# Performance work log

Measured on AMD Instinct MI355X. Metric: run time of the kernel, lower is better.

Reference implementation:

```python
import jax, jax.numpy as jnp
import numpy as np

NUM_HEADS = 16
HIDDEN = 1024
ATTN_DIM = 64            # per-head q/k dim
HEAD_OUT = 64            # per-head v dim
OUT_DIM = 1024
BATCH, SEQ = 2, 2048


def setup_inputs() -> dict:
    key = jax.random.key(0)
    ks = jax.random.split(key, 9)
    s_in = 1.0 / np.sqrt(HIDDEN)
    s_o = 1.0 / np.sqrt(NUM_HEADS * HEAD_OUT)
    return {
        "x": jax.random.normal(ks[0], (BATCH, SEQ, HIDDEN), dtype=jnp.float32),
        # Linear weights stored [in, out] so y = x @ W + b
        "Wq": jax.random.uniform(ks[1], (HIDDEN, NUM_HEADS * ATTN_DIM), jnp.float32, -s_in, s_in),
        "bq": jax.random.uniform(ks[2], (NUM_HEADS * ATTN_DIM,), jnp.float32, -s_in, s_in),
        "Wk": jax.random.uniform(ks[3], (HIDDEN, NUM_HEADS * ATTN_DIM), jnp.float32, -s_in, s_in),
        "bk": jax.random.uniform(ks[4], (NUM_HEADS * ATTN_DIM,), jnp.float32, -s_in, s_in),
        "Wv": jax.random.uniform(ks[5], (HIDDEN, NUM_HEADS * HEAD_OUT), jnp.float32, -s_in, s_in),
        "bv": jax.random.uniform(ks[6], (HIDDEN, NUM_HEADS * HEAD_OUT)[1:], jnp.float32, -s_in, s_in),
        "Wo": jax.random.uniform(ks[7], (NUM_HEADS * HEAD_OUT, OUT_DIM), jnp.float32, -s_o, s_o),
        "bo": jax.random.uniform(ks[8], (OUT_DIM,), jnp.float32, -s_o, s_o),
    }


def _split_heads(y, h):
    b, s, _ = y.shape
    return y.reshape(b, s, h, -1).transpose(0, 2, 1, 3)  # [b, h, s, d]


def reference(x, Wq, bq, Wk, bk, Wv, bv, Wo, bo):
    h = NUM_HEADS
    q = _split_heads(x @ Wq + bq, h)                    # [b,h,s,dq]
    k = _split_heads(x @ Wk + bk, h)                    # [b,h,s,dq]
    v = _split_heads(x @ Wv + bv, h)                    # [b,h,s,dv]
    scale = 1.0 / jnp.sqrt(jnp.float32(ATTN_DIM))
    # pattern[b,h,i,j] = key_i . query_j  (i=key index, j=query index)
    pattern = jnp.einsum('bhid,bhjd->bhij', k, q) * scale
    # softmax over key axis (dim=-2), matching t.softmax(..., dim=-2)
    prob = jax.nn.softmax(pattern, axis=-2)             # [b,h,key,query]
    # out[b,h,s,d] = sum_i prob[b,h,i,s] * v[b,h,i,d]
    out = jnp.einsum('bhis,bhid->bhsd', prob, v)        # [b,h,s,dv]
    b, _, s, dv = out.shape
    concat = out.transpose(0, 2, 1, 3).reshape(b, s, h * dv)
    return concat @ Wo + bo
```

## Files before the change

kernel.cpp:

```cpp
#include <hip/hip_runtime.h>
#include <cstdint>
#include <cstddef>

using f16   = _Float16;
using f16x4 = __attribute__((ext_vector_type(4))) _Float16;
using f16x8 = __attribute__((ext_vector_type(8))) _Float16;
using f32x4 = __attribute__((ext_vector_type(4))) float;

__device__ __forceinline__ f32x4 mfma16(f16x8 a, f16x8 b, f32x4 c) {
  return __builtin_amdgcn_mfma_f32_16x16x32_f16(a, b, c, 0, 0, 0);
}

__device__ __forceinline__ void gld16(const f16* g, f16* l) {
  __builtin_amdgcn_global_load_lds(
      (__attribute__((address_space(1))) void*)g,
      (__attribute__((address_space(3))) void*)l, 16, 0, 0);
}

constexpr int BATCH = 2, SEQL = 2048, HID = 1024, NH = 16, DH = 64;
constexpr int TOK = BATCH * SEQL;
constexpr int NQKV = 3 * HID;

__global__ __launch_bounds__(256) void k_convert_x(const float* __restrict__ x,
                                                   f16* __restrict__ xh) {
  int i = (blockIdx.x * 256 + threadIdx.x) * 4;
  float4 v = *(const float4*)(x + i);
  f16x4 o = { (f16)v.x, (f16)v.y, (f16)v.z, (f16)v.w };
  *(f16x4*)(xh + i) = o;
}

__global__ __launch_bounds__(256) void k_transpose(const float* __restrict__ Wq,
                                                   const float* __restrict__ Wk,
                                                   const float* __restrict__ Wv,
                                                   const float* __restrict__ Wo,
                                                   f16* __restrict__ WT,
                                                   f16* __restrict__ WoT) {
  __shared__ float tile[32][33];
  int mat = blockIdx.z;
  const float* W = (mat == 0) ? Wq : (mat == 1) ? Wk : (mat == 2) ? Wv : Wo;
  int in0 = blockIdx.x * 32, out0 = blockIdx.y * 32;
  int c = threadIdx.x & 31, r8 = threadIdx.x >> 5;
#pragma unroll
  for (int i = 0; i < 4; i++) {
    int r = r8 + i * 8;
    tile[r][c] = W[(size_t)(in0 + r) * HID + out0 + c];
  }
  __syncthreads();
#pragma unroll
  for (int i = 0; i < 4; i++) {
    int r = r8 + i * 8;
    f16 v = (f16)tile[c][r];
    if (mat == 3) WoT[(size_t)(out0 + r) * HID + in0 + c] = v;
    else          WT[(size_t)(mat * HID + out0 + r) * HID + in0 + c] = v;
  }
}

__global__ __launch_bounds__(256, 2) void k_gemm_qkv(
    const f16* __restrict__ xh, const f16* __restrict__ WT,
    const float* __restrict__ bq, const float* __restrict__ bk,
    const float* __restrict__ bv,
    f16* __restrict__ Qh, f16* __restrict__ Kh, f16* __restrict__ Vp) {
  constexpr int K = HID;
  int m0 = blockIdx.x * 128, n0 = blockIdx.y * 128;
  int tid = threadIdx.x;
  int w = tid >> 6, lane = tid & 63, lr = lane & 15, lq = lane >> 4;
  int wm = w >> 1, wn = w & 1;
  __shared__ f16 Ash[128 * 32];
  __shared__ f16 Bsh[128 * 32];
  f32x4 acc[4][4];
#pragma unroll
  for (int i = 0; i < 4; i++)
#pragma unroll
    for (int j = 0; j < 4; j++) acc[i][j] = (f32x4){0.f, 0.f, 0.f, 0.f};

  int row0 = tid >> 2, seg0 = tid & 3;
  int row1 = (256 + tid) >> 2;
  const f16* Ag0 = xh + (size_t)(m0 + row0) * K + seg0 * 8;
  const f16* Ag1 = xh + (size_t)(m0 + row1) * K + seg0 * 8;
  const f16* Bg0 = WT + (size_t)(n0 + row0) * K + seg0 * 8;
  const f16* Bg1 = WT + (size_t)(n0 + row1) * K + seg0 * 8;

  for (int k0 = 0; k0 < K; k0 += 32) {
    __syncthreads();
    gld16(Ag0 + k0, Ash + tid * 8);
    gld16(Ag1 + k0, Ash + (256 + tid) * 8);
    gld16(Bg0 + k0, Bsh + tid * 8);
    gld16(Bg1 + k0, Bsh + (256 + tid) * 8);
    __syncthreads();
    f16x8 af[4], bfr[4];
#pragma unroll
    for (int mt = 0; mt < 4; mt++)
      af[mt] = *(const f16x8*)(Ash + (wm * 64 + mt * 16 + lr) * 32 + lq * 8);
#pragma unroll
    for (int nt = 0; nt < 4; nt++)
      bfr[nt] = *(const f16x8*)(Bsh + (wn * 64 + nt * 16 + lr) * 32 + lq * 8);
#pragma unroll
    for (int mt = 0; mt < 4; mt++)
#pragma unroll
      for (int nt = 0; nt < 4; nt++)
        acc[mt][nt] = mfma16(af[mt], bfr[nt], acc[mt][nt]);
  }

#pragma unroll
  for (int nt = 0; nt < 4; nt++) {
    int o = n0 + wn * 64 + nt * 16 + lr;
    int sec = o >> 10, o1 = o & 1023, hh = o1 >> 6, dd = o1 & 63;
    float bias = (sec == 0) ? bq[o1] : (sec == 1) ? bk[o1] : bv[o1];
#pragma unroll
    for (int mt = 0; mt < 4; mt++) {
      int t0 = m0 + wm * 64 + mt * 16 + lq * 4;
      int b = t0 >> 11, s0 = t0 & (SEQL - 1);
      size_t bh = (size_t)(b * NH + hh);
      if (sec == 2) {
        f16x4 pv = { (f16)(acc[mt][nt][0] + bias), (f16)(acc[mt][nt][1] + bias),
                     (f16)(acc[mt][nt][2] + bias), (f16)(acc[mt][nt][3] + bias) };
        int pb = (s0 & ~31) | ((s0 & 12) << 1) | ((s0 >> 2) & 4);
        *(f16x4*)(Vp + (bh * DH + dd) * SEQL + pb) = pv;
      } else {
        f16* dst = (sec == 0) ? Qh : Kh;
#pragma unroll
        for (int r = 0; r < 4; r++)
          dst[(bh * SEQL + s0 + r) * DH + dd] = (f16)(acc[mt][nt][r] + bias);
      }
    }
  }
}

__global__ __launch_bounds__(256, 1) void k_attn(const f16* __restrict__ Qh,
                                                 const f16* __restrict__ Kh,
                                                 const f16* __restrict__ Vp,
                                                 f16* __restrict__ Ao) {
  int bh = blockIdx.x;
  int qblk = blockIdx.y;
  int b = bh >> 4, h = bh & 15;
  int tid = threadIdx.x, w = tid >> 6, lane = tid & 63, lr = lane & 15, lq = lane >> 4;

  __shared__ f16 Ksh[2][64 * 72];
  __shared__ f16 Vsh[2][64 * 72];

  f16x8 qf[4][2];
#pragma unroll
  for (int qt = 0; qt < 4; qt++) {
    const f16* Qbase =
        Qh + ((size_t)bh * SEQL + qblk * 256 + w * 64 + qt * 16 + lr) * DH;
#pragma unroll
    for (int ks = 0; ks < 2; ks++) {
      qf[qt][ks] = *(const f16x8*)(Qbase + ks * 32 + lq * 8);
      qf[qt][ks] = qf[qt][ks] * (f16)0.18033688f;
    }
  }

  f32x4 O[4][4];
#pragma unroll
  for (int qt = 0; qt < 4; qt++)
#pragma unroll
    for (int dt = 0; dt < 4; dt++) O[qt][dt] = (f32x4){0.f, 0.f, 0.f, 0.f};
  float lsum[4] = {0.f, 0.f, 0.f, 0.f};

  int srow = tid >> 3, sseg = tid & 7, srow1 = srow + 32;
  const f16* Kg0 = Kh + ((size_t)bh * SEQL + srow) * DH + sseg * 8;
  const f16* Kg1 = Kh + ((size_t)bh * SEQL + srow1) * DH + sseg * 8;
  const f16* Vg0 = Vp + ((size_t)bh * DH + srow) * SEQL + sseg * 8;
  const f16* Vg1 = Vp + ((size_t)bh * DH + srow1) * SEQL + sseg * 8;

  uint4 kr0 = *(const uint4*)(Kg0), kr1 = *(const uint4*)(Kg1);
  uint4 vr0 = *(const uint4*)(Vg0), vr1 = *(const uint4*)(Vg1);

  for (int kb = 0; kb < SEQL / 64; kb++) {
    f16* Kp = Ksh[kb & 1];
    f16* Vq = Vsh[kb & 1];
    *(uint4*)(Kp + srow * 72 + sseg * 8) = kr0;
    *(uint4*)(Kp + srow1 * 72 + sseg * 8) = kr1;
    *(uint4*)(Vq + srow * 72 + sseg * 8) = vr0;
    *(uint4*)(Vq + srow1 * 72 + sseg * 8) = vr1;
    if (kb < SEQL / 64 - 1) {
      size_t ko = (size_t)(kb + 1) * 64 * DH;
      int vo = (kb + 1) * 64;
      kr0 = *(const uint4*)(Kg0 + ko);
      kr1 = *(const uint4*)(Kg1 + ko);
      vr0 = *(const uint4*)(Vg0 + vo);
      vr1 = *(const uint4*)(Vg1 + vo);
    }
    __syncthreads();

    f32x4 sacc[4][4];
#pragma unroll
    for (int qt = 0; qt < 4; qt++)
#pragma unroll
      for (int kt = 0; kt < 4; kt++) sacc[qt][kt] = (f32x4){0.f, 0.f, 0.f, 0.f};
#pragma unroll
    for (int ks = 0; ks < 2; ks++) {
#pragma unroll
      for (int kt = 0; kt < 4; kt++) {
        f16x8 kf = *(const f16x8*)(Kp + (kt * 16 + lr) * 72 + ks * 32 + lq * 8);
        sacc[0][kt] = mfma16(kf, qf[0][ks], sacc[0][kt]);
        sacc[1][kt] = mfma16(kf, qf[1][ks], sacc[1][kt]);
        sacc[2][kt] = mfma16(kf, qf[2][ks], sacc[2][kt]);
        sacc[3][kt] = mfma16(kf, qf[3][ks], sacc[3][kt]);
      }
    }

    f16x8 pf[4][2];
#pragma unroll
    for (int qt = 0; qt < 4; qt++) {
      float part = 0.f;
#pragma unroll
      for (int kt = 0; kt < 4; kt++) {
        float p0 = __builtin_amdgcn_exp2f(sacc[qt][kt][0]);
        float p1 = __builtin_amdgcn_exp2f(sacc[qt][kt][1]);
        float p2 = __builtin_amdgcn_exp2f(sacc[qt][kt][2]);
        float p3 = __builtin_amdgcn_exp2f(sacc[qt][kt][3]);
        part += (p0 + p1) + (p2 + p3);
        int s = kt >> 1, off = (kt & 1) * 4;
        pf[qt][s][off + 0] = (f16)p0; pf[qt][s][off + 1] = (f16)p1;
        pf[qt][s][off + 2] = (f16)p2; pf[qt][s][off + 3] = (f16)p3;
      }
      lsum[qt] += part;
    }

#pragma unroll
    for (int s = 0; s < 2; s++) {
#pragma unroll
      for (int dt = 0; dt < 4; dt++) {
        f16x8 vf = *(const f16x8*)(Vq + (dt * 16 + lr) * 72 + s * 32 + lq * 8);
        O[0][dt] = mfma16(vf, pf[0][s], O[0][dt]);
        O[1][dt] = mfma16(vf, pf[1][s], O[1][dt]);
        O[2][dt] = mfma16(vf, pf[2][s], O[2][dt]);
        O[3][dt] = mfma16(vf, pf[3][s], O[3][dt]);
      }
    }
  }

#pragma unroll
  for (int qt = 0; qt < 4; qt++) {
    float l1 = lsum[qt] + __shfl_xor(lsum[qt], 16);
    float ltot = l1 + __shfl_xor(l1, 32);
    float inv = 1.0f / ltot;
    int q = qblk * 256 + w * 64 + qt * 16 + lr;
    f16* dst = Ao + ((size_t)b * SEQL + q) * HID + h * DH;
#pragma unroll
    for (int dt = 0; dt < 4; dt++) {
      f16x4 o = { (f16)(O[qt][dt][0] * inv), (f16)(O[qt][dt][1] * inv),
                  (f16)(O[qt][dt][2] * inv), (f16)(O[qt][dt][3] * inv) };
      *(f16x4*)(dst + dt * 16 + lq * 4) = o;
    }
  }
}

__global__ __launch_bounds__(256, 2) void k_gemm_out(const f16* __restrict__ Ah,
                                                     const f16* __restrict__ WoT,
                                                     const float* __restrict__ bo,
                                                     float* __restrict__ out) {
  constexpr int K = HID;
  int m0 = blockIdx.x * 128, n0 = blockIdx.y * 64;
  int tid = threadIdx.x;
  int w = tid >> 6, lane = tid & 63, lr = lane & 15, lq = lane >> 4;
  int wm = w >> 1, wn = w & 1;
  __shared__ f16 Ash[128 * 32];
  __shared__ f16 Bsh[64 * 32];
  f32x4 acc[4][2];
#pragma unroll
  for (int i = 0; i < 4; i++)
#pragma unroll
    for (int j = 0; j < 2; j++) acc[i][j] = (f32x4){0.f, 0.f, 0.f, 0.f};

  int row0 = tid >> 2, seg0 = tid & 3;
  int row1 = (256 + tid) >> 2;
  const f16* Ag0 = Ah + (size_t)(m0 + row0) * K + seg0 * 8;
  const f16* Ag1 = Ah + (size_t)(m0 + row1) * K + seg0 * 8;
  const f16* Bg0 = WoT + (size_t)(n0 + row0) * K + seg0 * 8;

  for (int k0 = 0; k0 < K; k0 += 32) {
    __syncthreads();
    gld16(Ag0 + k0, Ash + tid * 8);
    gld16(Ag1 + k0, Ash + (256 + tid) * 8);
    gld16(Bg0 + k0, Bsh + tid * 8);
    __syncthreads();
    f16x8 af[4], bfr[2];
#pragma unroll
    for (int mt = 0; mt < 4; mt++)
      af[mt] = *(const f16x8*)(Ash + (wm * 64 + mt * 16 + lr) * 32 + lq * 8);
#pragma unroll
    for (int nt = 0; nt < 2; nt++)
      bfr[nt] = *(const f16x8*)(Bsh + (wn * 32 + nt * 16 + lr) * 32 + lq * 8);
#pragma unroll
    for (int mt = 0; mt < 4; mt++)
#pragma unroll
      for (int nt = 0; nt < 2; nt++)
        acc[mt][nt] = mfma16(af[mt], bfr[nt], acc[mt][nt]);
  }

#pragma unroll
  for (int nt = 0; nt < 2; nt++) {
    int o = n0 + wn * 32 + nt * 16 + lr;
    float bias = bo[o];
#pragma unroll
    for (int mt = 0; mt < 4; mt++) {
      int t0 = m0 + wm * 64 + mt * 16 + lq * 4;
#pragma unroll
      for (int r = 0; r < 4; r++)
        out[(size_t)(t0 + r) * HID + o] = acc[mt][nt][r] + bias;
    }
  }
}

extern "C" void kernel_launch(void* const* d_in, const int* in_sizes, int n_in,
                              void* d_out, int out_size, void* d_ws, size_t ws_size,
                              hipStream_t stream) {
  const float* x  = (const float*)d_in[0];
  const float* Wq = (const float*)d_in[1];
  const float* bq = (const float*)d_in[2];
  const float* Wk = (const float*)d_in[3];
  const float* bk = (const float*)d_in[4];
  const float* Wv = (const float*)d_in[5];
  const float* bv = (const float*)d_in[6];
  const float* Wo = (const float*)d_in[7];
  const float* bo = (const float*)d_in[8];

  char* ws = (char*)d_ws;
  f16* xh  = (f16*)(ws + 0);
  f16* WT  = (f16*)(ws + 8388608);
  f16* WoT = (f16*)(ws + 14680064);
  f16* Qh  = (f16*)(ws + 16777216);
  f16* Kh  = (f16*)(ws + 25165824);
  f16* Vp  = (f16*)(ws + 33554432);
  f16* Ao  = (f16*)(ws + 41943040);

  k_convert_x<<<TOK * HID / 1024, 256, 0, stream>>>(x, xh);
  k_transpose<<<dim3(32, 32, 4), 256, 0, stream>>>(Wq, Wk, Wv, Wo, WT, WoT);
  k_gemm_qkv<<<dim3(TOK / 128, NQKV / 128), 256, 0, stream>>>(xh, WT, bq, bk, bv,
                                                              Qh, Kh, Vp);
  k_attn<<<dim3(BATCH * NH, SEQL / 256), 256, 0, stream>>>(Qh, Kh, Vp, Ao);
  k_gemm_out<<<dim3(TOK / 128, HID / 64), 256, 0, stream>>>(Ao, WoT, bo,
                                                            (float*)d_out);
}
```

Baseline: 193.1 us.

## Split attention key range across two wave groups per block and merge in LDS

The attention kernel now launches 512 threads per block. Two groups of four waves each handle half of the key sequence for the same 256 queries, and each group has its own double-buffered K/V tiles in shared memory. Partial outputs and row sums from the second group go through LDS, using an XOR-swizzled layout, and the first group combines them, normalizes and writes the result. With only 256 blocks in the grid, the aim is to double the waves per CU to hide latency better. The cost is a larger LDS footprint, block-wide syncs across both groups, and an extra reduction step at the end.

```diff
diff --git a/kernel.cpp b/kernel.cpp
--- a/kernel.cpp
+++ b/kernel.cpp
@@ -126,23 +126,26 @@
   }
 }
 
-__global__ __launch_bounds__(256, 1) void k_attn(const f16* __restrict__ Qh,
+__global__ __launch_bounds__(512, 2) void k_attn(const f16* __restrict__ Qh,
                                                  const f16* __restrict__ Kh,
                                                  const f16* __restrict__ Vp,
                                                  f16* __restrict__ Ao) {
   int bh = blockIdx.x;
   int qblk = blockIdx.y;
   int b = bh >> 4, h = bh & 15;
-  int tid = threadIdx.x, w = tid >> 6, lane = tid & 63, lr = lane & 15, lq = lane >> 4;
-
-  __shared__ f16 Ksh[2][64 * 72];
-  __shared__ f16 Vsh[2][64 * 72];
+  int tid = threadIdx.x;
+  int w = tid >> 6;
+  int g = w >> 2;
+  int wq = w & 3;
+  int lane = tid & 63, lr = lane & 15, lq = lane >> 4;
+
+  __shared__ f16 sh[8 * 64 * 72];
 
   f16x8 qf[4][2];
 #pragma unroll
   for (int qt = 0; qt < 4; qt++) {
     const f16* Qbase =
-        Qh + ((size_t)bh * SEQL + qblk * 256 + w * 64 + qt * 16 + lr) * DH;
+        Qh + ((size_t)bh * SEQL + qblk * 256 + wq * 64 + qt * 16 + lr) * DH;
 #pragma unroll
     for (int ks = 0; ks < 2; ks++) {
       qf[qt][ks] = *(const f16x8*)(Qbase + ks * 32 + lq * 8);
@@ -157,23 +160,25 @@
     for (int dt = 0; dt < 4; dt++) O[qt][dt] = (f32x4){0.f, 0.f, 0.f, 0.f};
   float lsum[4] = {0.f, 0.f, 0.f, 0.f};
 
-  int srow = tid >> 3, sseg = tid & 7, srow1 = srow + 32;
-  const f16* Kg0 = Kh + ((size_t)bh * SEQL + srow) * DH + sseg * 8;
-  const f16* Kg1 = Kh + ((size_t)bh * SEQL + srow1) * DH + sseg * 8;
-  const f16* Vg0 = Vp + ((size_t)bh * DH + srow) * SEQL + sseg * 8;
-  const f16* Vg1 = Vp + ((size_t)bh * DH + srow1) * SEQL + sseg * 8;
+  int gtid = tid & 255;
+  int srow = gtid >> 3, sseg = gtid & 7, srow1 = srow + 32;
+  int kbase = g * 1024;
+  const f16* Kg0 = Kh + ((size_t)bh * SEQL + kbase + srow) * DH + sseg * 8;
+  const f16* Kg1 = Kh + ((size_t)bh * SEQL + kbase + srow1) * DH + sseg * 8;
+  const f16* Vg0 = Vp + ((size_t)bh * DH + srow) * SEQL + kbase + sseg * 8;
+  const f16* Vg1 = Vp + ((size_t)bh * DH + srow1) * SEQL + kbase + sseg * 8;
 
   uint4 kr0 = *(const uint4*)(Kg0), kr1 = *(const uint4*)(Kg1);
   uint4 vr0 = *(const uint4*)(Vg0), vr1 = *(const uint4*)(Vg1);
 
-  for (int kb = 0; kb < SEQL / 64; kb++) {
-    f16* Kp = Ksh[kb & 1];
-    f16* Vq = Vsh[kb & 1];
+  for (int kb = 0; kb < 16; kb++) {
+    f16* Kp = sh + ((g * 2 + (kb & 1)) * 2 + 0) * 4608;
+    f16* Vq = Kp + 4608;
     *(uint4*)(Kp + srow * 72 + sseg * 8) = kr0;
     *(uint4*)(Kp + srow1 * 72 + sseg * 8) = kr1;
     *(uint4*)(Vq + srow * 72 + sseg * 8) = vr0;
     *(uint4*)(Vq + srow1 * 72 + sseg * 8) = vr1;
-    if (kb < SEQL / 64 - 1) {
+    if (kb < 15) {
       size_t ko = (size_t)(kb + 1) * 64 * DH;
       int vo = (kb + 1) * 64;
       kr0 = *(const uint4*)(Kg0 + ko);
@@ -231,18 +236,42 @@
     }
   }
 
-#pragma unroll
-  for (int qt = 0; qt < 4; qt++) {
-    float l1 = lsum[qt] + __shfl_xor(lsum[qt], 16);
-    float ltot = l1 + __shfl_xor(l1, 32);
-    float inv = 1.0f / ltot;
-    int q = qblk * 256 + w * 64 + qt * 16 + lr;
-    f16* dst = Ao + ((size_t)b * SEQL + q) * HID + h * DH;
-#pragma unroll
-    for (int dt = 0; dt < 4; dt++) {
-      f16x4 o = { (f16)(O[qt][dt][0] * inv), (f16)(O[qt][dt][1] * inv),
-                  (f16)(O[qt][dt][2] * inv), (f16)(O[qt][dt][3] * inv) };
-      *(f16x4*)(dst + dt * 16 + lq * 4) = o;
+  __syncthreads();
+  float* part = (float*)sh;
+  float* plsum = part + 16384;
+  if (g == 1) {
+#pragma unroll
+    for (int qt = 0; qt < 4; qt++) {
+      int ql = wq * 64 + qt * 16 + lr;
+#pragma unroll
+      for (int dt = 0; dt < 4; dt++) {
+        int slot = (dt * 4 + lq) ^ lr;
+        *(f32x4*)(part + ql * 64 + slot * 4) = O[qt][dt];
+      }
+      plsum[ql * 4 + lq] = lsum[qt];
+    }
+  }
+  __syncthreads();
+  if (g == 0) {
+#pragma unroll
+    for (int qt = 0; qt < 4; qt++) {
+      int ql = wq * 64 + qt * 16 + lr;
+      float ls = lsum[qt] + plsum[ql * 4 + lq];
+      float l1 = ls + __shfl_xor(ls, 16);
+      float ltot = l1 + __shfl_xor(l1, 32);
+      float inv = 1.0f / ltot;
+      int q = qblk * 256 + ql;
+      f16* dst = Ao + ((size_t)b * SEQL + q) * HID + h * DH;
+#pragma unroll
+      for (int dt = 0; dt < 4; dt++) {
+        int slot = (dt * 4 + lq) ^ lr;
+        f32x4 po = *(const f32x4*)(part + ql * 64 + slot * 4);
+        f16x4 o = { (f16)((O[qt][dt][0] + po[0]) * inv),
+                    (f16)((O[qt][dt][1] + po[1]) * inv),
+                    (f16)((O[qt][dt][2] + po[2]) * inv),
+                    (f16)((O[qt][dt][3] + po[3]) * inv) };
+        *(f16x4*)(dst + dt * 16 + lq * 4) = o;
+      }
     }
   }
 }
@@ -330,7 +359,7 @@
   k_transpose<<<dim3(32, 32, 4), 256, 0, stream>>>(Wq, Wk, Wv, Wo, WT, WoT);
   k_gemm_qkv<<<dim3(TOK / 128, NQKV / 128), 256, 0, stream>>>(xh, WT, bq, bk, bv,
                                                               Qh, Kh, Vp);
-  k_attn<<<dim3(BATCH * NH, SEQL / 256), 256, 0, stream>>>(Qh, Kh, Vp, Ao);
+  k_attn<<<dim3(BATCH * NH, SEQL / 256), 512, 0, stream>>>(Qh, Kh, Vp, Ao);
   k_gemm_out<<<dim3(TOK / 128, HID / 64), 256, 0, stream>>>(Ao, WoT, bo,
                                                             (float*)d_out);
 }
```

After: 179.8 us. -6.9%, faster.
